# Kernel tuning notes

Hardware: AMD Instinct MI355X
Metric: run time of the kernel (lower is better)

## Reference

```python
import jax, jax.numpy as jnp
import numpy as np

N_DIMS, N_EMBD, N_LAYER = 64, 256, 12
B, N = 32, 1024
LN_EPS = 1e-5


def setup_inputs() -> dict:
    key = jax.random.key(0)
    ks = jax.random.split(key, 16)
    s = 0.02
    inp = {
        'xs': jax.random.normal(ks[0], (B, N, N_DIMS - 1), dtype=jnp.float32),
        'ys': jax.random.normal(ks[1], (B, N), dtype=jnp.float32),
        # read-in linear
        'W_in': jax.random.normal(ks[2], (N_DIMS, N_EMBD), dtype=jnp.float32) * s,
        'b_in': jnp.zeros((N_EMBD,), jnp.float32),
        # per-layer attention projections (no bias)
        'Wq': jax.random.normal(ks[3], (N_LAYER, N_EMBD, N_EMBD), dtype=jnp.float32) * s,
        'Wk': jax.random.normal(ks[4], (N_LAYER, N_EMBD, N_EMBD), dtype=jnp.float32) * s,
        'Wv': jax.random.normal(ks[5], (N_LAYER, N_EMBD, N_EMBD), dtype=jnp.float32) * s,
        # layernorm 1
        'g1': jnp.ones((N_LAYER, N_EMBD), jnp.float32),
        'be1': jnp.zeros((N_LAYER, N_EMBD), jnp.float32),
        # mlp: Linear -> ReLU -> Linear
        'W1': jax.random.normal(ks[6], (N_LAYER, N_EMBD, N_EMBD), dtype=jnp.float32) * s,
        'b1': jnp.zeros((N_LAYER, N_EMBD), jnp.float32),
        'W2': jax.random.normal(ks[7], (N_LAYER, N_EMBD, N_EMBD), dtype=jnp.float32) * s,
        'b2': jnp.zeros((N_LAYER, N_EMBD), jnp.float32),
        # layernorm 2
        'g2': jnp.ones((N_LAYER, N_EMBD), jnp.float32),
        'be2': jnp.zeros((N_LAYER, N_EMBD), jnp.float32),
        # read-out linear
        'W_out': jax.random.normal(ks[8], (N_EMBD, 1), dtype=jnp.float32) * s,
        'b_out': jnp.zeros((1,), jnp.float32),
    }
    return inp


def _layernorm(x, g, b):
    mu = jnp.mean(x, axis=-1, keepdims=True)
    var = jnp.mean(jnp.square(x - mu), axis=-1, keepdims=True)
    return (x - mu) * jax.lax.rsqrt(var + LN_EPS) * g + b


def reference(xs, ys, W_in, b_in, Wq, Wk, Wv, g1, be1, W1, b1, W2, b2, g2, be2, W_out, b_out):
    n = ys.shape[1]
    # _combine: zs [B, N, d+1], zero the y slot of the last (test) token
    zs = jnp.concatenate([xs, ys[:, :, None]], axis=2)
    zs = zs.at[:, -1, -1].set(0.0)
    H = zs @ W_in + b_in  # [B, N, E]
    for i in range(N_LAYER):
        q = H @ Wq[i]
        k = H @ Wk[i]
        v = H @ Wv[i]
        attn = jax.nn.relu(jnp.einsum('bid,bjd->bij', q, k)) / n
        H = H + jnp.einsum('bij,bjd->bid', attn, v)
        H = _layernorm(H, g1[i], be1[i])
        H = H + (jax.nn.relu(H @ W1[i] + b1[i]) @ W2[i] + b2[i])
        H = _layernorm(H, g2[i], be2[i])
    pred = H @ W_out + b_out  # [B, N, 1]
    return pred[:, :n, 0]  # default inds = arange(ys.shape[1])
```

## Files before the change

### kernel.cpp

```cpp
#include <hip/hip_runtime.h>
#include <math.h>

#define E 256
#define NTOK 1024
#define NB 32
#define NLAYER 12
#define LN_EPS 1e-5f

typedef __attribute__((ext_vector_type(8))) short bf16x8;
typedef __attribute__((ext_vector_type(4))) float f32x4;
#define MFMA16(a, b, c) __builtin_amdgcn_mfma_f32_16x16x32_bf16(a, b, c, 0, 0, 0)

__device__ __forceinline__ ushort f2bf(float f) {
    union { float f; unsigned u; } v; v.f = f;
    return (ushort)((v.u + 0x7fffu + ((v.u >> 16) & 1u)) >> 16);
}

__global__ __launch_bounds__(256) void k_wprep(
    const float* __restrict__ Wq, const float* __restrict__ Wk, const float* __restrict__ Wv,
    const float* __restrict__ W1, const float* __restrict__ W2,
    ushort* __restrict__ WT)
{
    const int mat = blockIdx.x % 5;
    const int l   = blockIdx.x / 5;
    const float* src = (mat == 0 ? Wq : mat == 1 ? Wk : mat == 2 ? Wv : mat == 3 ? W1 : W2)
                       + (size_t)l * E * E;
    ushort* dst = WT + ((size_t)(l * 5 + mat) << 16);
    const int n = threadIdx.x;
    #pragma unroll
    for (int c = 0; c < 4; ++c) {
        #pragma unroll
        for (int j = 0; j < 8; ++j) {
            const int k0 = c * 64 + j * 8;
            uint4 u;
            u.x = (uint)f2bf(src[(size_t)(k0 + 0) * E + n]) | ((uint)f2bf(src[(size_t)(k0 + 1) * E + n]) << 16);
            u.y = (uint)f2bf(src[(size_t)(k0 + 2) * E + n]) | ((uint)f2bf(src[(size_t)(k0 + 3) * E + n]) << 16);
            u.z = (uint)f2bf(src[(size_t)(k0 + 4) * E + n]) | ((uint)f2bf(src[(size_t)(k0 + 5) * E + n]) << 16);
            u.w = (uint)f2bf(src[(size_t)(k0 + 6) * E + n]) | ((uint)f2bf(src[(size_t)(k0 + 7) * E + n]) << 16);
            *(uint4*)&dst[(size_t)n * E + k0] = u;
        }
    }
}

__global__ __launch_bounds__(256) void k_embed(
    const float* __restrict__ xs, const float* __restrict__ ys,
    const float* __restrict__ W_in, const float* __restrict__ b_in,
    float* __restrict__ H, ushort* __restrict__ Hb)
{
    __shared__ float zs[16][64];
    const int tid = threadIdx.x;
    const int r0 = blockIdx.x * 16;
    #pragma unroll
    for (int l = 0; l < 4; ++l) {
        int lin = tid + l * 256;
        int i = lin >> 6, d = lin & 63;
        int row = r0 + i;
        int t = row & (NTOK - 1);
        float v;
        if (d < 63) v = xs[(size_t)row * 63 + d];
        else        v = (t == NTOK - 1) ? 0.f : ys[row];
        zs[i][d] = v;
    }
    __syncthreads();
    float acc[16];
    #pragma unroll
    for (int i = 0; i < 16; ++i) acc[i] = 0.f;
    for (int d = 0; d < 64; ++d) {
        float w = W_in[d * E + tid];
        #pragma unroll
        for (int i = 0; i < 16; ++i) acc[i] = fmaf(zs[i][d], w, acc[i]);
    }
    float bb = b_in[tid];
    #pragma unroll
    for (int i = 0; i < 16; ++i) {
        float o = acc[i] + bb;
        H [(size_t)(r0 + i) * E + tid] = o;
        Hb[(size_t)(r0 + i) * E + tid] = f2bf(o);
    }
}

__device__ __forceinline__ void qkv_gemm(
    const ushort* __restrict__ Wt, const ushort* __restrict__ Hb,
    size_t r0, int tid, int w, int lr, int lg,
    ushort (&Ws)[256][72], f32x4 (&acc)[4][4])
{
    #pragma unroll
    for (int mt = 0; mt < 4; ++mt)
        #pragma unroll
        for (int nt = 0; nt < 4; ++nt) acc[mt][nt] = (f32x4){0.f, 0.f, 0.f, 0.f};
    #pragma unroll 1
    for (int kc = 0; kc < 4; ++kc) {
        __syncthreads();
        #pragma unroll
        for (int rep = 0; rep < 8; ++rep) {
            int lin = rep * 256 + tid;
            int n = lin >> 3, slot = lin & 7;
            bf16x8 v = *(const bf16x8*)&Wt[(size_t)n * E + kc * 64 + slot * 8];
            *(bf16x8*)&Ws[n][slot * 8] = v;
        }
        __syncthreads();
        #pragma unroll
        for (int kl = 0; kl < 2; ++kl) {
            bf16x8 af[4], bw[4];
            #pragma unroll
            for (int mt = 0; mt < 4; ++mt)
                af[mt] = *(const bf16x8*)&Hb[(r0 + mt * 16 + lr) * E + kc * 64 + kl * 32 + lg * 8];
            #pragma unroll
            for (int nt = 0; nt < 4; ++nt)
                bw[nt] = *(const bf16x8*)&Ws[w * 64 + nt * 16 + lr][kl * 32 + lg * 8];
            #pragma unroll
            for (int mt = 0; mt < 4; ++mt)
                #pragma unroll
                for (int nt = 0; nt < 4; ++nt)
                    acc[mt][nt] = MFMA16(af[mt], bw[nt], acc[mt][nt]);
        }
    }
}

__device__ __forceinline__ void qkv_out_qk(
    ushort* __restrict__ Out, size_t r0, int w, int l, int lr, int lg,
    ushort (&ScW)[16][72], f32x4 (&acc)[4][4])
{
    #pragma unroll
    for (int mt = 0; mt < 4; ++mt) {
        #pragma unroll
        for (int nt = 0; nt < 4; ++nt)
            #pragma unroll
            for (int r = 0; r < 4; ++r)
                ScW[lg * 4 + r][nt * 16 + lr] = f2bf(acc[mt][nt][r]);
        #pragma unroll
        for (int j = 0; j < 2; ++j) {
            bf16x8 v = *(const bf16x8*)&ScW[l >> 2][(l & 3) * 16 + j * 8];
            *(bf16x8*)&Out[(r0 + mt * 16 + (l >> 2)) * E + w * 64 + (l & 3) * 16 + j * 8] = v;
        }
    }
}

__global__ __launch_bounds__(256, 2) void k_qkv(
    const ushort* __restrict__ Hb,
    const ushort* __restrict__ WqT, const ushort* __restrict__ WkT, const ushort* __restrict__ WvT,
    ushort* __restrict__ Qb, ushort* __restrict__ Kb, ushort* __restrict__ VTg)
{
    __shared__ __align__(16) ushort Ws[256][72];
    __shared__ __align__(16) ushort Sc[4][16][72];
    const int tid = threadIdx.x;
    const int w = tid >> 6, l = tid & 63;
    const int lr = l & 15, lg = l >> 4;
    const size_t r0 = (size_t)blockIdx.x * 64;
    const int b    = (int)(r0 >> 10);
    const int tok0 = (int)(r0 & (NTOK - 1));

    f32x4 acc[4][4];

    qkv_gemm(WqT, Hb, r0, tid, w, lr, lg, Ws, acc);
    qkv_out_qk(Qb, r0, w, l, lr, lg, Sc[w], acc);

    qkv_gemm(WkT, Hb, r0, tid, w, lr, lg, Ws, acc);
    qkv_out_qk(Kb, r0, w, l, lr, lg, Sc[w], acc);

    qkv_gemm(WvT, Hb, r0, tid, w, lr, lg, Ws, acc);
    __syncthreads();
    #pragma unroll
    for (int mt = 0; mt < 4; ++mt)
        #pragma unroll
        for (int nt = 0; nt < 4; ++nt) {
            ushort4 u;
            u.x = f2bf(acc[mt][nt][0]); u.y = f2bf(acc[mt][nt][1]);
            u.z = f2bf(acc[mt][nt][2]); u.w = f2bf(acc[mt][nt][3]);
            *(ushort4*)&Ws[w * 64 + nt * 16 + lr][mt * 16 + lg * 4] = u;
        }
    __syncthreads();
    #pragma unroll
    for (int rep = 0; rep < 8; ++rep) {
        int lin = rep * 256 + tid;
        int row = lin >> 3, ch = lin & 7;
        bf16x8 v = *(const bf16x8*)&Ws[row][ch * 8];
        *(bf16x8*)&VTg[((size_t)b * E + row) * NTOK + tok0 + ch * 8] = v;
    }
}

#define ATTN_LOAD_TILE(koff, ka, kb_, va_, vb_)                                          \
    ka  = *(const bf16x8*)&Kb [kvbase + (size_t)((koff) + (tid >> 5)) * E + (tid & 31) * 8];       \
    kb_ = *(const bf16x8*)&Kb [kvbase + (size_t)((koff) + 16 + (tid >> 5)) * E + (tid & 31) * 8];  \
    va_ = *(const bf16x8*)&VTg[vtbase + (size_t)(tid >> 2) * NTOK + (koff) + (tid & 3) * 8];       \
    vb_ = *(const bf16x8*)&VTg[vtbase + (size_t)(128 + (tid >> 2)) * NTOK + (koff) + (tid & 3) * 8];

__global__ __launch_bounds__(512, 2) void k_attn(
    const ushort* __restrict__ Qb, const ushort* __restrict__ Kb, const ushort* __restrict__ VTg,
    float* __restrict__ H, ushort* __restrict__ HbO,
    const float* __restrict__ g1, const float* __restrict__ be1)
{
    __shared__ __align__(16) ushort Ks[32][264];
    __shared__ __align__(16) ushort VT[256][40];
    __shared__ __align__(16) ushort Pl[8][16][40];
    const int tid = threadIdx.x;
    const int w  = tid >> 6, l = tid & 63;
    const int lr = l & 15, lg = l >> 4;

    const int bid   = blockIdx.x;
    const int batch = bid & 31;
    const int tile  = bid >> 5;

    const size_t kvbase = (size_t)batch * NTOK * E;
    const size_t vtbase = (size_t)batch * E * NTOK;
    const int    qrow0  = tile * 128 + w * 16;
    const size_t qbase  = kvbase + (size_t)qrow0 * E;

    bf16x8 qf[8];
    #pragma unroll
    for (int kk = 0; kk < 8; ++kk)
        qf[kk] = *(const bf16x8*)&Qb[qbase + (size_t)lr * E + kk * 32 + lg * 8];

    f32x4 o[16];
    #pragma unroll
    for (int nt = 0; nt < 16; ++nt) o[nt] = (f32x4){0.f, 0.f, 0.f, 0.f};

    const float inv_n = 1.0f / (float)NTOK;
    const int wsw = ((lg >> 1) & 1) << 3;
    const int rsw = ((lr >> 3) & 1) << 3;

    bf16x8 cka, ckb, cva, cvb;
    ATTN_LOAD_TILE(0, cka, ckb, cva, cvb);

    #pragma unroll 1
    for (int jt = 0; jt < 32; ++jt) {
        __syncthreads();
        *(bf16x8*)&Ks[ 0 + (tid >> 5)][(tid & 31) * 8] = cka;
        *(bf16x8*)&Ks[16 + (tid >> 5)][(tid & 31) * 8] = ckb;
        *(bf16x8*)&VT[  0 + (tid >> 2)][(tid & 3) * 8] = cva;
        *(bf16x8*)&VT[128 + (tid >> 2)][(tid & 3) * 8] = cvb;
        bf16x8 nka, nkb, nva, nvb;
        {
            const int kn = ((jt + 1) & 31) * 32;
            ATTN_LOAD_TILE(kn, nka, nkb, nva, nvb);
        }
        __syncthreads();

        f32x4 s0 = (f32x4){0.f, 0.f, 0.f, 0.f};
        f32x4 s1 = (f32x4){0.f, 0.f, 0.f, 0.f};
        #pragma unroll
        for (int kk = 0; kk < 8; ++kk) {
            bf16x8 b0 = *(const bf16x8*)&Ks[lr][kk * 32 + lg * 8];
            bf16x8 b1 = *(const bf16x8*)&Ks[16 + lr][kk * 32 + lg * 8];
            s0 = MFMA16(qf[kk], b0, s0);
            s1 = MFMA16(qf[kk], b1, s1);
        }
        #pragma unroll
        for (int r = 0; r < 4; ++r) {
            Pl[w][lg * 4 + r][lr ^ wsw]        = f2bf(fmaxf(s0[r], 0.f) * inv_n);
            Pl[w][lg * 4 + r][(16 + lr) ^ wsw] = f2bf(fmaxf(s1[r], 0.f) * inv_n);
        }
        bf16x8 pa = *(const bf16x8*)&Pl[w][lr][(lg * 8) ^ rsw];
        #pragma unroll
        for (int nt = 0; nt < 16; ++nt) {
            bf16x8 vb = *(const bf16x8*)&VT[nt * 16 + lr][lg * 8];
            o[nt] = MFMA16(pa, vb, o[nt]);
        }
        cka = nka; ckb = nkb; cva = nva; cvb = nvb;
    }

    float gg[16], bb[16];
    #pragma unroll
    for (int nt = 0; nt < 16; ++nt) {
        gg[nt] = g1[nt * 16 + lr];
        bb[nt] = be1[nt * 16 + lr];
    }
    #pragma unroll
    for (int r = 0; r < 4; ++r) {
        const int q = lg * 4 + r;
        const size_t rowbase = kvbase + (size_t)(qrow0 + q) * E;
        float xv[16];
        float s = 0.f, s2 = 0.f;
        #pragma unroll
        for (int nt = 0; nt < 16; ++nt) {
            float val = H[rowbase + nt * 16 + lr] + o[nt][r];
            xv[nt] = val;
            s += val; s2 += val * val;
        }
        #pragma unroll
        for (int m = 1; m < 16; m <<= 1) {
            s  += __shfl_xor(s, m, 64);
            s2 += __shfl_xor(s2, m, 64);
        }
        float mu = s * (1.f / 256.f);
        float rs = rsqrtf(s2 * (1.f / 256.f) - mu * mu + LN_EPS);
        #pragma unroll
        for (int nt = 0; nt < 16; ++nt) {
            float ov = (xv[nt] - mu) * rs * gg[nt] + bb[nt];
            H  [rowbase + nt * 16 + lr] = ov;
            HbO[rowbase + nt * 16 + lr] = f2bf(ov);
        }
    }
}

__global__ __launch_bounds__(256, 2) void k_mlp(
    const ushort* __restrict__ Hb, float* __restrict__ H, ushort* __restrict__ HbO,
    const ushort* __restrict__ W1T, const float* __restrict__ b1,
    const ushort* __restrict__ W2T, const float* __restrict__ b2,
    const float* __restrict__ g2, const float* __restrict__ be2)
{
    __shared__ __align__(16) ushort Ws[256][72];
    __shared__ __align__(16) ushort Ts[64][264];
    __shared__ float part[4][64][2];
    __shared__ float stats[64][2];
    const int tid = threadIdx.x;
    const int w = tid >> 6, l = tid & 63;
    const int lr = l & 15, lg = l >> 4;
    const size_t r0 = (size_t)blockIdx.x * 64;

    f32x4 acc[4][4];
    qkv_gemm(W1T, Hb, r0, tid, w, lr, lg, Ws, acc);
    {
        float bb1[4];
        #pragma unroll
        for (int nt = 0; nt < 4; ++nt) bb1[nt] = b1[w * 64 + nt * 16 + lr];
        #pragma unroll
        for (int mt = 0; mt < 4; ++mt)
            #pragma unroll
            for (int nt = 0; nt < 4; ++nt)
                #pragma unroll
                for (int r = 0; r < 4; ++r)
                    Ts[mt * 16 + lg * 4 + r][w * 64 + nt * 16 + lr]
                        = f2bf(fmaxf(acc[mt][nt][r] + bb1[nt], 0.f));
    }

    f32x4 acc2[4][4];
    #pragma unroll
    for (int mt = 0; mt < 4; ++mt)
        #pragma unroll
        for (int nt = 0; nt < 4; ++nt) acc2[mt][nt] = (f32x4){0.f, 0.f, 0.f, 0.f};
    #pragma unroll 1
    for (int kc = 0; kc < 4; ++kc) {
        __syncthreads();
        #pragma unroll
        for (int rep = 0; rep < 8; ++rep) {
            int lin = rep * 256 + tid;
            int n = lin >> 3, slot = lin & 7;
            bf16x8 v = *(const bf16x8*)&W2T[(size_t)n * E + kc * 64 + slot * 8];
            *(bf16x8*)&Ws[n][slot * 8] = v;
        }
        __syncthreads();
        #pragma unroll
        for (int kl = 0; kl < 2; ++kl) {
            bf16x8 af[4], bw[4];
            #pragma unroll
            for (int mt = 0; mt < 4; ++mt)
                af[mt] = *(const bf16x8*)&Ts[mt * 16 + lr][kc * 64 + kl * 32 + lg * 8];
            #pragma unroll
            for (int nt = 0; nt < 4; ++nt)
                bw[nt] = *(const bf16x8*)&Ws[w * 64 + nt * 16 + lr][kl * 32 + lg * 8];
            #pragma unroll
            for (int mt = 0; mt < 4; ++mt)
                #pragma unroll
                for (int nt = 0; nt < 4; ++nt)
                    acc2[mt][nt] = MFMA16(af[mt], bw[nt], acc2[mt][nt]);
        }
    }

    {
        float b2v[4];
        #pragma unroll
        for (int nt = 0; nt < 4; ++nt) b2v[nt] = b2[w * 64 + nt * 16 + lr];
        #pragma unroll
        for (int mt = 0; mt < 4; ++mt)
            #pragma unroll
            for (int r = 0; r < 4; ++r)
                #pragma unroll
                for (int nt = 0; nt < 4; ++nt)
                    acc2[mt][nt][r] += H[(r0 + mt * 16 + lg * 4 + r) * E + w * 64 + nt * 16 + lr]
                                       + b2v[nt];
    }
    #pragma unroll
    for (int mt = 0; mt < 4; ++mt)
        #pragma unroll
        for (int r = 0; r < 4; ++r) {
            float s = 0.f, s2 = 0.f;
            #pragma unroll
            for (int nt = 0; nt < 4; ++nt) {
                float v = acc2[mt][nt][r];
                s += v; s2 += v * v;
            }
            #pragma unroll
            for (int m = 1; m < 16; m <<= 1) {
                s  += __shfl_xor(s, m, 64);
                s2 += __shfl_xor(s2, m, 64);
            }
            if (lr == 0) {
                part[w][mt * 16 + lg * 4 + r][0] = s;
                part[w][mt * 16 + lg * 4 + r][1] = s2;
            }
        }
    __syncthreads();
    if (tid < 64) {
        float s = part[0][tid][0] + part[1][tid][0] + part[2][tid][0] + part[3][tid][0];
        float s2 = part[0][tid][1] + part[1][tid][1] + part[2][tid][1] + part[3][tid][1];
        float mu = s * (1.f / 256.f);
        stats[tid][0] = mu;
        stats[tid][1] = rsqrtf(s2 * (1.f / 256.f) - mu * mu + LN_EPS);
    }
    __syncthreads();
    {
        float gg[4], be[4];
        #pragma unroll
        for (int nt = 0; nt < 4; ++nt) {
            gg[nt] = g2[w * 64 + nt * 16 + lr];
            be[nt] = be2[w * 64 + nt * 16 + lr];
        }
        #pragma unroll
        for (int mt = 0; mt < 4; ++mt)
            #pragma unroll
            for (int r = 0; r < 4; ++r) {
                const int row = mt * 16 + lg * 4 + r;
                const float mu = stats[row][0], rs = stats[row][1];
                const size_t rowbase = (r0 + row) * E;
                #pragma unroll
                for (int nt = 0; nt < 4; ++nt) {
                    float ov = (acc2[mt][nt][r] - mu) * rs * gg[nt] + be[nt];
                    H  [rowbase + w * 64 + nt * 16 + lr] = ov;
                    HbO[rowbase + w * 64 + nt * 16 + lr] = f2bf(ov);
                }
            }
    }
}

__global__ __launch_bounds__(256) void k_readout(
    const float* __restrict__ H, const float* __restrict__ W_out,
    const float* __restrict__ b_out, float* __restrict__ out)
{
    const int tid = threadIdx.x;
    const int lane = tid & 63;
    const int row = blockIdx.x * 4 + (tid >> 6);
    float s = 0.f;
    #pragma unroll
    for (int j = 0; j < 4; ++j)
        s += H[(size_t)row * E + j * 64 + lane] * W_out[j * 64 + lane];
    #pragma unroll
    for (int m = 1; m < 64; m <<= 1) s += __shfl_xor(s, m, 64);
    if (lane == 0) out[row] = s + b_out[0];
}

extern "C" void kernel_launch(void* const* d_in, const int* in_sizes, int n_in,
                              void* d_out, int out_size, void* d_ws, size_t ws_size,
                              hipStream_t stream)
{
    const float* xs    = (const float*)d_in[0];
    const float* ys    = (const float*)d_in[1];
    const float* W_in  = (const float*)d_in[2];
    const float* b_in  = (const float*)d_in[3];
    const float* Wq    = (const float*)d_in[4];
    const float* Wk    = (const float*)d_in[5];
    const float* Wv    = (const float*)d_in[6];
    const float* g1    = (const float*)d_in[7];
    const float* be1   = (const float*)d_in[8];
    const float* W1    = (const float*)d_in[9];
    const float* b1    = (const float*)d_in[10];
    const float* W2    = (const float*)d_in[11];
    const float* b2    = (const float*)d_in[12];
    const float* g2    = (const float*)d_in[13];
    const float* be2   = (const float*)d_in[14];
    const float* W_out = (const float*)d_in[15];
    const float* b_out = (const float*)d_in[16];
    (void)in_sizes; (void)n_in; (void)out_size; (void)ws_size;

    const size_t SZ = (size_t)NB * NTOK * E;
    float*  H   = (float*)d_ws;
    ushort* Hb  = (ushort*)(H + SZ);
    ushort* Qb  = Hb + SZ;
    ushort* Kb  = Qb + SZ;
    ushort* VTg = Kb + SZ;
    ushort* WT  = VTg + SZ;

    k_wprep<<<dim3(NLAYER * 5), dim3(256), 0, stream>>>(Wq, Wk, Wv, W1, W2, WT);
    k_embed<<<dim3(2048), dim3(256), 0, stream>>>(xs, ys, W_in, b_in, H, Hb);
    for (int i = 0; i < NLAYER; ++i) {
        const size_t vo = (size_t)i * E;
        const ushort* WqT = WT + ((size_t)(i * 5 + 0) << 16);
        const ushort* WkT = WT + ((size_t)(i * 5 + 1) << 16);
        const ushort* WvT = WT + ((size_t)(i * 5 + 2) << 16);
        const ushort* W1T = WT + ((size_t)(i * 5 + 3) << 16);
        const ushort* W2T = WT + ((size_t)(i * 5 + 4) << 16);
        k_qkv<<<dim3(512), dim3(256), 0, stream>>>(Hb, WqT, WkT, WvT, Qb, Kb, VTg);
        k_attn<<<dim3(256), dim3(512), 0, stream>>>(Qb, Kb, VTg, H, Hb, g1 + vo, be1 + vo);
        k_mlp<<<dim3(512), dim3(256), 0, stream>>>(Hb, H, Hb, W1T, b1 + vo, W2T, b2 + vo,
                                                   g2 + vo, be2 + vo);
    }
    k_readout<<<dim3((NB * NTOK) / 4), dim3(256), 0, stream>>>(H, W_out, b_out, (float*)d_out);
}
```

Baseline: 1.731 ms.

## Halve attention block size to 64 query rows and raise MFMA wave priority

The attention kernel now uses 256-thread blocks, each covering 64 query rows, launched as 512 blocks instead of 256 blocks of 512 threads. Each thread therefore loads and stores four K and four V chunks per tile instead of two. The MFMA compute section is also wrapped in s_setprio(1)/s_setprio(0) so waves doing math get scheduling priority over waves issuing loads. More blocks may fill the 256 CUs better and improve latency hiding, but each K/V tile is staged per 64 queries instead of 128, so total K/V global traffic doubles and each thread holds more prefetch registers.

```diff
diff --git a/kernel.cpp b/kernel.cpp
--- a/kernel.cpp
+++ b/kernel.cpp
@@ -179,20 +179,14 @@
     }
 }
 
-#define ATTN_LOAD_TILE(koff, ka, kb_, va_, vb_)                                          \
-    ka  = *(const bf16x8*)&Kb [kvbase + (size_t)((koff) + (tid >> 5)) * E + (tid & 31) * 8];       \
-    kb_ = *(const bf16x8*)&Kb [kvbase + (size_t)((koff) + 16 + (tid >> 5)) * E + (tid & 31) * 8];  \
-    va_ = *(const bf16x8*)&VTg[vtbase + (size_t)(tid >> 2) * NTOK + (koff) + (tid & 3) * 8];       \
-    vb_ = *(const bf16x8*)&VTg[vtbase + (size_t)(128 + (tid >> 2)) * NTOK + (koff) + (tid & 3) * 8];
-
-__global__ __launch_bounds__(512, 2) void k_attn(
+__global__ __launch_bounds__(256, 2) void k_attn(
     const ushort* __restrict__ Qb, const ushort* __restrict__ Kb, const ushort* __restrict__ VTg,
     float* __restrict__ H, ushort* __restrict__ HbO,
     const float* __restrict__ g1, const float* __restrict__ be1)
 {
     __shared__ __align__(16) ushort Ks[32][264];
     __shared__ __align__(16) ushort VT[256][40];
-    __shared__ __align__(16) ushort Pl[8][16][40];
+    __shared__ __align__(16) ushort Pl[4][16][40];
     const int tid = threadIdx.x;
     const int w  = tid >> 6, l = tid & 63;
     const int lr = l & 15, lg = l >> 4;
@@ -203,7 +197,7 @@
 
     const size_t kvbase = (size_t)batch * NTOK * E;
     const size_t vtbase = (size_t)batch * E * NTOK;
-    const int    qrow0  = tile * 128 + w * 16;
+    const int    qrow0  = tile * 64 + w * 16;
     const size_t qbase  = kvbase + (size_t)qrow0 * E;
 
     bf16x8 qf[8];
@@ -219,23 +213,47 @@
     const int wsw = ((lg >> 1) & 1) << 3;
     const int rsw = ((lr >> 3) & 1) << 3;
 
-    bf16x8 cka, ckb, cva, cvb;
-    ATTN_LOAD_TILE(0, cka, ckb, cva, cvb);
+    const int krow = tid >> 5, kch = tid & 31;
+    const int vrow = tid >> 2, vch = tid & 3;
+
+    bf16x8 ck0, ck1, ck2, ck3, cv0, cv1, cv2, cv3;
+    {
+        ck0 = *(const bf16x8*)&Kb[kvbase + (size_t)( 0 + krow) * E + kch * 8];
+        ck1 = *(const bf16x8*)&Kb[kvbase + (size_t)( 8 + krow) * E + kch * 8];
+        ck2 = *(const bf16x8*)&Kb[kvbase + (size_t)(16 + krow) * E + kch * 8];
+        ck3 = *(const bf16x8*)&Kb[kvbase + (size_t)(24 + krow) * E + kch * 8];
+        cv0 = *(const bf16x8*)&VTg[vtbase + (size_t)(  0 + vrow) * NTOK + vch * 8];
+        cv1 = *(const bf16x8*)&VTg[vtbase + (size_t)( 64 + vrow) * NTOK + vch * 8];
+        cv2 = *(const bf16x8*)&VTg[vtbase + (size_t)(128 + vrow) * NTOK + vch * 8];
+        cv3 = *(const bf16x8*)&VTg[vtbase + (size_t)(192 + vrow) * NTOK + vch * 8];
+    }
 
     #pragma unroll 1
     for (int jt = 0; jt < 32; ++jt) {
         __syncthreads();
-        *(bf16x8*)&Ks[ 0 + (tid >> 5)][(tid & 31) * 8] = cka;
-        *(bf16x8*)&Ks[16 + (tid >> 5)][(tid & 31) * 8] = ckb;
-        *(bf16x8*)&VT[  0 + (tid >> 2)][(tid & 3) * 8] = cva;
-        *(bf16x8*)&VT[128 + (tid >> 2)][(tid & 3) * 8] = cvb;
-        bf16x8 nka, nkb, nva, nvb;
+        *(bf16x8*)&Ks[ 0 + krow][kch * 8] = ck0;
+        *(bf16x8*)&Ks[ 8 + krow][kch * 8] = ck1;
+        *(bf16x8*)&Ks[16 + krow][kch * 8] = ck2;
+        *(bf16x8*)&Ks[24 + krow][kch * 8] = ck3;
+        *(bf16x8*)&VT[  0 + vrow][vch * 8] = cv0;
+        *(bf16x8*)&VT[ 64 + vrow][vch * 8] = cv1;
+        *(bf16x8*)&VT[128 + vrow][vch * 8] = cv2;
+        *(bf16x8*)&VT[192 + vrow][vch * 8] = cv3;
+        bf16x8 nk0, nk1, nk2, nk3, nv0, nv1, nv2, nv3;
         {
             const int kn = ((jt + 1) & 31) * 32;
-            ATTN_LOAD_TILE(kn, nka, nkb, nva, nvb);
+            nk0 = *(const bf16x8*)&Kb[kvbase + (size_t)(kn +  0 + krow) * E + kch * 8];
+            nk1 = *(const bf16x8*)&Kb[kvbase + (size_t)(kn +  8 + krow) * E + kch * 8];
+            nk2 = *(const bf16x8*)&Kb[kvbase + (size_t)(kn + 16 + krow) * E + kch * 8];
+            nk3 = *(const bf16x8*)&Kb[kvbase + (size_t)(kn + 24 + krow) * E + kch * 8];
+            nv0 = *(const bf16x8*)&VTg[vtbase + (size_t)(  0 + vrow) * NTOK + kn + vch * 8];
+            nv1 = *(const bf16x8*)&VTg[vtbase + (size_t)( 64 + vrow) * NTOK + kn + vch * 8];
+            nv2 = *(const bf16x8*)&VTg[vtbase + (size_t)(128 + vrow) * NTOK + kn + vch * 8];
+            nv3 = *(const bf16x8*)&VTg[vtbase + (size_t)(192 + vrow) * NTOK + kn + vch * 8];
         }
         __syncthreads();
 
+        __builtin_amdgcn_s_setprio(1);
         f32x4 s0 = (f32x4){0.f, 0.f, 0.f, 0.f};
         f32x4 s1 = (f32x4){0.f, 0.f, 0.f, 0.f};
         #pragma unroll
@@ -256,7 +274,9 @@
             bf16x8 vb = *(const bf16x8*)&VT[nt * 16 + lr][lg * 8];
             o[nt] = MFMA16(pa, vb, o[nt]);
         }
-        cka = nka; ckb = nkb; cva = nva; cvb = nvb;
+        __builtin_amdgcn_s_setprio(0);
+        ck0 = nk0; ck1 = nk1; ck2 = nk2; ck3 = nk3;
+        cv0 = nv0; cv1 = nv1; cv2 = nv2; cv3 = nv3;
     }
 
     float gg[16], bb[16];
@@ -480,7 +500,7 @@
         const ushort* W1T = WT + ((size_t)(i * 5 + 3) << 16);
         const ushort* W2T = WT + ((size_t)(i * 5 + 4) << 16);
         k_qkv<<<dim3(512), dim3(256), 0, stream>>>(Hb, WqT, WkT, WvT, Qb, Kb, VTg);
-        k_attn<<<dim3(256), dim3(512), 0, stream>>>(Qb, Kb, VTg, H, Hb, g1 + vo, be1 + vo);
+        k_attn<<<dim3(512), dim3(256), 0, stream>>>(Qb, Kb, VTg, H, Hb, g1 + vo, be1 + vo);
         k_mlp<<<dim3(512), dim3(256), 0, stream>>>(Hb, H, Hb, W1T, b1 + vo, W2T, b2 + vo,
                                                    g2 + vo, be2 + vo);
     }
```

After: 1.772 ms. +2.3%, slower.
